# Kernel optimization log

Measured on AMD Instinct MI355X. Metric: run time of the kernel, lower is better.

The kernel has to match this reference:

```python
import jax, jax.numpy as jnp
import numpy as np
from jax import lax


def setup_inputs() -> dict:
    key = jax.random.key(0)
    k1, k2, k3 = jax.random.split(key, 3)
    B, P, D = 4, 64, 768
    N, R = 2048, 12
    positions = jax.random.normal(k1, (B, P, D), dtype=jnp.float32)
    # module inits keys with std=0.01 (we use randn*0.01); adjacency is a learned
    # dense R x N x N parameter (init zeros in source -> use small noise so the
    # read path is non-degenerate for kernel correctness checks)
    keys_param = jax.random.normal(k2, (N, D), dtype=jnp.float32) * 0.01
    adjacency = jax.random.normal(k3, (R, N, N), dtype=jnp.float32) * 0.01
    return {"positions": positions, "keys_param": keys_param,
            "adjacency": adjacency, "k": 16}


def reference(positions, keys_param, adjacency, k):
    # keys property: L2-normalize along feature dim
    keys = keys_param * lax.rsqrt(
        jnp.sum(keys_param * keys_param, axis=-1, keepdims=True) + 1e-12)

    # anchor: key matching scores = positions . keys^T  -> (B, P, N)
    scores = jnp.einsum('bpd,nd->bpn', positions, keys)

    # topk_sparse addressing: keep top-k nodes per position, normalize to sum 1
    vals, idx = lax.top_k(scores, k)           # (B, P, k)
    w = jax.nn.softmax(vals, axis=-1)          # normalized anchor weights

    # read: position -> node -> (rel, nei_node), honoring top-k sparsity by
    # gathering only the k selected adjacency rows per relation (no dense BPN matmul)
    adj_rows = adjacency[:, idx, :]            # (R, B, P, k, N) gather
    nei = jnp.einsum('bpk,rbpkn->bpn', w, adj_rows)   # neighbor node scores

    # project neighbor node distribution back through keys -> (B, P, D)
    out = jnp.einsum('bpn,nd->bpd', nei, keys)
    return out
```

## Files before the change

### kernel.cpp

```cpp
#include <hip/hip_runtime.h>
#include <math.h>

#define B_ 4
#define P_ 64
#define D_ 768
#define N_ 2048
#define R_ 12
#define K_ 16
#define Q_ 256
#define SPLITS_ 8
#define BK_ 32

__global__ __launch_bounds__(256) void k_norm(const float* __restrict__ kp,
                                              float* __restrict__ keys) {
    int row = blockIdx.x;
    int tid = threadIdx.x;
    const float* src = kp + (size_t)row * D_;
    float x0 = src[tid], x1 = src[tid + 256], x2 = src[tid + 512];
    float ss = x0 * x0 + x1 * x1 + x2 * x2;
    #pragma unroll
    for (int off = 32; off > 0; off >>= 1) ss += __shfl_down(ss, off, 64);
    __shared__ float sm[4];
    if ((tid & 63) == 0) sm[tid >> 6] = ss;
    __syncthreads();
    float tot = sm[0] + sm[1] + sm[2] + sm[3];
    float inv = 1.0f / sqrtf(tot + 1e-12f);
    float* dst = keys + (size_t)row * D_;
    dst[tid] = x0 * inv;
    dst[tid + 256] = x1 * inv;
    dst[tid + 512] = x2 * inv;
}

__global__ __launch_bounds__(256) void k_scores(const float* __restrict__ pos,
                                                const float* __restrict__ keys,
                                                float* __restrict__ scores) {
    __shared__ float Ast[BK_][68];
    __shared__ float Bst[BK_][68];
    int tid = threadIdx.x;
    int tx = tid & 15, ty = tid >> 4;
    int n0 = blockIdx.x * 64, q0 = blockIdx.y * 64;
    float acc[4][4] = {};
    for (int kb = 0; kb < D_; kb += BK_) {
        #pragma unroll
        for (int e = 0; e < 2; e++) {
            int elem = tid + e * 256;
            int row = elem >> 3, c4 = elem & 7;
            float4 v = *(const float4*)(pos + (size_t)(q0 + row) * D_ + kb + c4 * 4);
            Ast[c4 * 4 + 0][row] = v.x; Ast[c4 * 4 + 1][row] = v.y;
            Ast[c4 * 4 + 2][row] = v.z; Ast[c4 * 4 + 3][row] = v.w;
        }
        #pragma unroll
        for (int e = 0; e < 2; e++) {
            int elem = tid + e * 256;
            int row = elem >> 3, c4 = elem & 7;
            float4 v = *(const float4*)(keys + (size_t)(n0 + row) * D_ + kb + c4 * 4);
            Bst[c4 * 4 + 0][row] = v.x; Bst[c4 * 4 + 1][row] = v.y;
            Bst[c4 * 4 + 2][row] = v.z; Bst[c4 * 4 + 3][row] = v.w;
        }
        __syncthreads();
        #pragma unroll 4
        for (int kk = 0; kk < BK_; kk++) {
            float4 a = *(const float4*)&Ast[kk][ty * 4];
            float4 b = *(const float4*)&Bst[kk][tx * 4];
            float av[4] = {a.x, a.y, a.z, a.w};
            float bv[4] = {b.x, b.y, b.z, b.w};
            #pragma unroll
            for (int i = 0; i < 4; i++)
                #pragma unroll
                for (int j = 0; j < 4; j++)
                    acc[i][j] += av[i] * bv[j];
        }
        __syncthreads();
    }
    #pragma unroll
    for (int i = 0; i < 4; i++) {
        float4 v = {acc[i][0], acc[i][1], acc[i][2], acc[i][3]};
        *(float4*)(scores + (size_t)(q0 + ty * 4 + i) * N_ + n0 + tx * 4) = v;
    }
}

__global__ __launch_bounds__(256) void k_topk(const float* __restrict__ scores,
                                              float* __restrict__ wout,
                                              int* __restrict__ iout) {
    int q = blockIdx.x, tid = threadIdx.x;
    __shared__ float s[N_];
    __shared__ float rv[4];
    __shared__ int ri[4];
    __shared__ float lv[K_];
    __shared__ int li[K_];
    #pragma unroll
    for (int i = 0; i < 8; i++) s[tid + i * 256] = scores[(size_t)q * N_ + tid + i * 256];
    __syncthreads();
    for (int r = 0; r < K_; r++) {
        float bv = -3.0e38f;
        int bi = 0;
        #pragma unroll
        for (int i = 0; i < 8; i++) {
            int j = tid + i * 256;
            float v = s[j];
            if (v > bv) { bv = v; bi = j; }
        }
        #pragma unroll
        for (int off = 32; off > 0; off >>= 1) {
            float ov = __shfl_down(bv, off, 64);
            int oi = __shfl_down(bi, off, 64);
            if (ov > bv || (ov == bv && oi < bi)) { bv = ov; bi = oi; }
        }
        if ((tid & 63) == 0) { rv[tid >> 6] = bv; ri[tid >> 6] = bi; }
        __syncthreads();
        if (tid == 0) {
            float mv = rv[0];
            int mi = ri[0];
            for (int w2 = 1; w2 < 4; w2++)
                if (rv[w2] > mv || (rv[w2] == mv && ri[w2] < mi)) { mv = rv[w2]; mi = ri[w2]; }
            lv[r] = mv; li[r] = mi;
            s[mi] = -3.0e38f;
        }
        __syncthreads();
    }
    if (tid == 0) {
        float m = lv[0];
        float e[K_];
        float sum = 0.f;
        for (int i = 0; i < K_; i++) { e[i] = expf(lv[i] - m); sum += e[i]; }
        float isum = 1.0f / sum;
        for (int i = 0; i < K_; i++) {
            wout[q * K_ + i] = e[i] * isum;
            iout[q * K_ + i] = li[i];
        }
    }
}

__global__ __launch_bounds__(256) void k_asum(const float* __restrict__ adj,
                                              float* __restrict__ asum) {
    size_t i = (size_t)blockIdx.x * 256 + threadIdx.x;
    const float4* a4 = (const float4*)adj;
    const size_t plane = (size_t)N_ * N_ / 4;
    float4 acc = {0.f, 0.f, 0.f, 0.f};
    #pragma unroll
    for (int r = 0; r < R_; r++) {
        float4 v = a4[(size_t)r * plane + i];
        acc.x += v.x; acc.y += v.y; acc.z += v.z; acc.w += v.w;
    }
    ((float4*)asum)[i] = acc;
}

__global__ __launch_bounds__(256) void k_nei(const float* __restrict__ asum,
                                             const float* __restrict__ wv,
                                             const int* __restrict__ iv,
                                             float* __restrict__ nei) {
    int q = blockIdx.x, tid = threadIdx.x;
    __shared__ float wi[K_];
    __shared__ int ii[K_];
    if (tid < K_) { wi[tid] = wv[q * K_ + tid]; ii[tid] = iv[q * K_ + tid]; }
    __syncthreads();
    float4 acc0 = {0.f, 0.f, 0.f, 0.f};
    float4 acc1 = {0.f, 0.f, 0.f, 0.f};
    #pragma unroll
    for (int k = 0; k < K_; k++) {
        const float4* row = (const float4*)(asum + (size_t)ii[k] * N_);
        float wk = wi[k];
        float4 v0 = row[tid], v1 = row[tid + 256];
        acc0.x += wk * v0.x; acc0.y += wk * v0.y; acc0.z += wk * v0.z; acc0.w += wk * v0.w;
        acc1.x += wk * v1.x; acc1.y += wk * v1.y; acc1.z += wk * v1.z; acc1.w += wk * v1.w;
    }
    float4* dst = (float4*)(nei + (size_t)q * N_);
    dst[tid] = acc0;
    dst[tid + 256] = acc1;
}

__global__ __launch_bounds__(256) void k_out_part(const float* __restrict__ nei,
                                                  const float* __restrict__ keys,
                                                  float* __restrict__ part) {
    __shared__ float Ast[BK_][68];
    __shared__ float Bst[BK_][68];
    int tid = threadIdx.x;
    int tx = tid & 15, ty = tid >> 4;
    int d0 = blockIdx.x * 64;
    int q0 = blockIdx.y * 64;
    int z = blockIdx.z;
    float acc[4][4] = {};
    for (int kb = z * (N_ / SPLITS_); kb < (z + 1) * (N_ / SPLITS_); kb += BK_) {
        #pragma unroll
        for (int e = 0; e < 2; e++) {
            int elem = tid + e * 256;
            int row = elem >> 3, c4 = elem & 7;
            float4 v = *(const float4*)(nei + (size_t)(q0 + row) * N_ + kb + c4 * 4);
            Ast[c4 * 4 + 0][row] = v.x; Ast[c4 * 4 + 1][row] = v.y;
            Ast[c4 * 4 + 2][row] = v.z; Ast[c4 * 4 + 3][row] = v.w;
        }
        #pragma unroll
        for (int e = 0; e < 2; e++) {
            int elem = tid + e * 256;
            int kr = elem >> 4, c4 = elem & 15;
            float4 v = *(const float4*)(keys + (size_t)(kb + kr) * D_ + d0 + c4 * 4);
            *(float4*)&Bst[kr][c4 * 4] = v;
        }
        __syncthreads();
        #pragma unroll 4
        for (int kk = 0; kk < BK_; kk++) {
            float4 a = *(const float4*)&Ast[kk][ty * 4];
            float4 b = *(const float4*)&Bst[kk][tx * 4];
            float av[4] = {a.x, a.y, a.z, a.w};
            float bv[4] = {b.x, b.y, b.z, b.w};
            #pragma unroll
            for (int i = 0; i < 4; i++)
                #pragma unroll
                for (int j = 0; j < 4; j++)
                    acc[i][j] += av[i] * bv[j];
        }
        __syncthreads();
    }
    float* base = part + (size_t)z * Q_ * D_;
    #pragma unroll
    for (int i = 0; i < 4; i++) {
        float4 v = {acc[i][0], acc[i][1], acc[i][2], acc[i][3]};
        *(float4*)(base + (size_t)(q0 + ty * 4 + i) * D_ + d0 + tx * 4) = v;
    }
}

__global__ __launch_bounds__(256) void k_reduce(const float* __restrict__ part,
                                                float* __restrict__ out) {
    int i = blockIdx.x * 256 + threadIdx.x;
    const float4* p4 = (const float4*)part;
    const int plane = Q_ * D_ / 4;
    float4 acc = {0.f, 0.f, 0.f, 0.f};
    #pragma unroll
    for (int z = 0; z < SPLITS_; z++) {
        float4 v = p4[(size_t)z * plane + i];
        acc.x += v.x; acc.y += v.y; acc.z += v.z; acc.w += v.w;
    }
    ((float4*)out)[i] = acc;
}

extern "C" void kernel_launch(void* const* d_in, const int* in_sizes, int n_in,
                              void* d_out, int out_size, void* d_ws, size_t ws_size,
                              hipStream_t stream) {
    const float* pos = (const float*)d_in[0];
    const float* kp  = (const float*)d_in[1];
    const float* adj = (const float*)d_in[2];
    float* out = (float*)d_out;

    float* ws     = (float*)d_ws;
    float* keys   = ws;
    float* asum   = keys + (size_t)N_ * D_;
    float* scores = asum + (size_t)N_ * N_;
    float* nei    = scores + (size_t)Q_ * N_;
    float* wbuf   = nei + (size_t)Q_ * N_;
    int*   ibuf   = (int*)(wbuf + Q_ * K_);
    float* part   = asum;

    k_norm<<<N_, 256, 0, stream>>>(kp, keys);
    k_scores<<<dim3(32, 4), 256, 0, stream>>>(pos, keys, scores);
    k_topk<<<Q_, 256, 0, stream>>>(scores, wbuf, ibuf);
    k_asum<<<4096, 256, 0, stream>>>(adj, asum);
    k_nei<<<Q_, 256, 0, stream>>>(asum, wbuf, ibuf, nei);
    k_out_part<<<dim3(12, 4, SPLITS_), 256, 0, stream>>>(nei, keys, part);
    k_reduce<<<192, 256, 0, stream>>>(part, out);
}
```

Before: 409.5 us.

## Split score GEMM over D and rewrite top-k as per-wave register selection

The scores GEMM is split into two halves along the feature dimension, which doubles the grid from 128 to 256 blocks, and the two partial score buffers are summed inside the top-k kernel. Top-k now keeps values in registers: each wave finds its own local top-16 with xor shuffles and no block barriers, and then one wave merges the 64 candidates and computes the softmax in parallel across lanes. This removes the 32 __syncthreads per row and the serial tid==0 work, at the cost of an extra partial-score buffer write and read. The total runtime is probably dominated by the adjacency sum over 200MB, so the overall effect is limited.

```diff
diff --git a/kernel.cpp b/kernel.cpp
--- a/kernel.cpp
+++ b/kernel.cpp
@@ -10,6 +10,7 @@
 #define Q_ 256
 #define SPLITS_ 8
 #define BK_ 32
+#define NEG_INF_ -3.0e38f
 
 __global__ __launch_bounds__(256) void k_norm(const float* __restrict__ kp,
                                               float* __restrict__ keys) {
@@ -33,14 +34,15 @@
 
 __global__ __launch_bounds__(256) void k_scores(const float* __restrict__ pos,
                                                 const float* __restrict__ keys,
-                                                float* __restrict__ scores) {
+                                                float* __restrict__ spart) {
     __shared__ float Ast[BK_][68];
     __shared__ float Bst[BK_][68];
     int tid = threadIdx.x;
     int tx = tid & 15, ty = tid >> 4;
     int n0 = blockIdx.x * 64, q0 = blockIdx.y * 64;
+    int z = blockIdx.z;
     float acc[4][4] = {};
-    for (int kb = 0; kb < D_; kb += BK_) {
+    for (int kb = z * (D_ / 2); kb < (z + 1) * (D_ / 2); kb += BK_) {
         #pragma unroll
         for (int e = 0; e < 2; e++) {
             int elem = tid + e * 256;
@@ -72,61 +74,76 @@
         }
         __syncthreads();
     }
+    float* base = spart + (size_t)z * Q_ * N_;
     #pragma unroll
     for (int i = 0; i < 4; i++) {
         float4 v = {acc[i][0], acc[i][1], acc[i][2], acc[i][3]};
-        *(float4*)(scores + (size_t)(q0 + ty * 4 + i) * N_ + n0 + tx * 4) = v;
-    }
-}
-
-__global__ __launch_bounds__(256) void k_topk(const float* __restrict__ scores,
+        *(float4*)(base + (size_t)(q0 + ty * 4 + i) * N_ + n0 + tx * 4) = v;
+    }
+}
+
+__global__ __launch_bounds__(256) void k_topk(const float* __restrict__ s0,
+                                              const float* __restrict__ s1,
                                               float* __restrict__ wout,
                                               int* __restrict__ iout) {
     int q = blockIdx.x, tid = threadIdx.x;
-    __shared__ float s[N_];
-    __shared__ float rv[4];
-    __shared__ int ri[4];
-    __shared__ float lv[K_];
-    __shared__ int li[K_];
-    #pragma unroll
-    for (int i = 0; i < 8; i++) s[tid + i * 256] = scores[(size_t)q * N_ + tid + i * 256];
+    int w = tid >> 6, lane = tid & 63;
+    int base = w * 512 + lane;
+    const float* r0 = s0 + (size_t)q * N_;
+    const float* r1 = s1 + (size_t)q * N_;
+    float v[8];
+    #pragma unroll
+    for (int j = 0; j < 8; j++) {
+        int n = base + j * 64;
+        v[j] = r0[n] + r1[n];
+    }
+    __shared__ float cv[64];
+    __shared__ int ci[64];
+    for (int r = 0; r < K_; r++) {
+        float bv = NEG_INF_;
+        int bi = 0;
+        #pragma unroll
+        for (int j = 0; j < 8; j++) {
+            int n = base + j * 64;
+            if (v[j] > bv) { bv = v[j]; bi = n; }
+        }
+        #pragma unroll
+        for (int off = 1; off < 64; off <<= 1) {
+            float ov = __shfl_xor(bv, off, 64);
+            int oi = __shfl_xor(bi, off, 64);
+            if (ov > bv || (ov == bv && oi < bi)) { bv = ov; bi = oi; }
+        }
+        if (lane == 0) { cv[w * K_ + r] = bv; ci[w * K_ + r] = bi; }
+        #pragma unroll
+        for (int j = 0; j < 8; j++)
+            if (base + j * 64 == bi) v[j] = NEG_INF_;
+    }
     __syncthreads();
-    for (int r = 0; r < K_; r++) {
-        float bv = -3.0e38f;
-        int bi = 0;
-        #pragma unroll
-        for (int i = 0; i < 8; i++) {
-            int j = tid + i * 256;
-            float v = s[j];
-            if (v > bv) { bv = v; bi = j; }
-        }
-        #pragma unroll
-        for (int off = 32; off > 0; off >>= 1) {
-            float ov = __shfl_down(bv, off, 64);
-            int oi = __shfl_down(bi, off, 64);
-            if (ov > bv || (ov == bv && oi < bi)) { bv = ov; bi = oi; }
-        }
-        if ((tid & 63) == 0) { rv[tid >> 6] = bv; ri[tid >> 6] = bi; }
-        __syncthreads();
-        if (tid == 0) {
-            float mv = rv[0];
-            int mi = ri[0];
-            for (int w2 = 1; w2 < 4; w2++)
-                if (rv[w2] > mv || (rv[w2] == mv && ri[w2] < mi)) { mv = rv[w2]; mi = ri[w2]; }
-            lv[r] = mv; li[r] = mi;
-            s[mi] = -3.0e38f;
-        }
-        __syncthreads();
-    }
-    if (tid == 0) {
-        float m = lv[0];
-        float e[K_];
-        float sum = 0.f;
-        for (int i = 0; i < K_; i++) { e[i] = expf(lv[i] - m); sum += e[i]; }
-        float isum = 1.0f / sum;
-        for (int i = 0; i < K_; i++) {
-            wout[q * K_ + i] = e[i] * isum;
-            iout[q * K_ + i] = li[i];
+    if (w == 0) {
+        float mv = cv[lane];
+        int mi = ci[lane];
+        float sel_v = NEG_INF_;
+        int sel_i = 0;
+        for (int r = 0; r < K_; r++) {
+            float bv = mv;
+            int bi = mi;
+            #pragma unroll
+            for (int off = 1; off < 64; off <<= 1) {
+                float ov = __shfl_xor(bv, off, 64);
+                int oi = __shfl_xor(bi, off, 64);
+                if (ov > bv || (ov == bv && oi < bi)) { bv = ov; bi = oi; }
+            }
+            if (lane == r) { sel_v = bv; sel_i = bi; }
+            if (mi == bi) mv = NEG_INF_;
+        }
+        float m = __shfl(sel_v, 0, 64);
+        float e = (lane < K_) ? expf(sel_v - m) : 0.0f;
+        float sum = e;
+        #pragma unroll
+        for (int off = 1; off < 64; off <<= 1) sum += __shfl_xor(sum, off, 64);
+        if (lane < K_) {
+            wout[q * K_ + lane] = e / sum;
+            iout[q * K_ + lane] = sel_i;
         }
     }
 }
@@ -244,15 +261,15 @@
     float* ws     = (float*)d_ws;
     float* keys   = ws;
     float* asum   = keys + (size_t)N_ * D_;
-    float* scores = asum + (size_t)N_ * N_;
-    float* nei    = scores + (size_t)Q_ * N_;
+    float* spart  = asum + (size_t)N_ * N_;
+    float* nei    = spart + 2 * (size_t)Q_ * N_;
     float* wbuf   = nei + (size_t)Q_ * N_;
     int*   ibuf   = (int*)(wbuf + Q_ * K_);
     float* part   = asum;
 
     k_norm<<<N_, 256, 0, stream>>>(kp, keys);
-    k_scores<<<dim3(32, 4), 256, 0, stream>>>(pos, keys, scores);
-    k_topk<<<Q_, 256, 0, stream>>>(scores, wbuf, ibuf);
+    k_scores<<<dim3(32, 4, 2), 256, 0, stream>>>(pos, keys, spart);
+    k_topk<<<Q_, 256, 0, stream>>>(spart, spart + (size_t)Q_ * N_, wbuf, ibuf);
     k_asum<<<4096, 256, 0, stream>>>(adj, asum);
     k_nei<<<Q_, 256, 0, stream>>>(asum, wbuf, ibuf, nei);
     k_out_part<<<dim3(12, 4, SPLITS_), 256, 0, stream>>>(nei, keys, part);
```

After: 386.2 us. 1.06x faster.
